# Kernel tuning notes

Measured on AMD Instinct MI355X. Metric: run time of the kernel, lower is better.

## Reference

```python
import jax, jax.numpy as jnp
import numpy as np

DIM = 1024
N_HEADS = 16
HEAD_DIM = DIM // N_HEADS


def setup_inputs() -> dict:
    key = jax.random.key(0)
    k1, k2, k3 = jax.random.split(key, 3)
    x = jax.random.normal(k1, (1, 4096, DIM), dtype=jnp.float32)
    # nn.Linear weights stored as [out, in]; y = x @ W.T
    w_qkv = jax.random.normal(k2, (3 * DIM, DIM), dtype=jnp.float32) * (DIM ** -0.5)
    w_o = jax.random.normal(k3, (DIM, DIM), dtype=jnp.float32) * (DIM ** -0.5)
    return {"x": x, "w_qkv": w_qkv, "w_o": w_o}


def reference(x, w_qkv, w_o):
    b, s, _ = x.shape
    qkv = jnp.einsum('bsd,ed->bse', x, w_qkv)  # [b, s, 3*dim]
    qkv = qkv.reshape(b, s, 3, N_HEADS, HEAD_DIM)
    qkv = jnp.transpose(qkv, (2, 0, 3, 1, 4))  # [3, b, h, s, hd]
    q, k, v = qkv[0], qkv[1], qkv[2]
    scale = HEAD_DIM ** -0.5
    scores = jnp.einsum('bhqd,bhkd->bhqk', q, k) * scale  # full O(N^2) scores
    attn = jax.nn.softmax(scores, axis=-1)
    out = jnp.einsum('bhqk,bhkd->bhqd', attn, v)
    out = jnp.transpose(out, (0, 2, 1, 3)).reshape(b, s, DIM)
    return jnp.einsum('bsd,ed->bse', out, w_o)
```

## Files before the change

kernel.cpp:

```cpp
#include <hip/hip_runtime.h>

typedef __bf16 bf16x8 __attribute__((ext_vector_type(8)));
typedef float f32x4 __attribute__((ext_vector_type(4)));
typedef unsigned short ushort_t;
typedef unsigned int uint_t;

constexpr int S = 4096, DMODEL = 1024, NH = 16, HD = 64;
#define QSCALE 0.18033688011112042f

#if __has_builtin(__builtin_amdgcn_exp2f)
#define EXP2(x) __builtin_amdgcn_exp2f(x)
#else
#define EXP2(x) exp2f(x)
#endif

__device__ inline ushort_t f2bf(float f) {
  uint_t u = __builtin_bit_cast(uint_t, f);
  u = u + 0x7FFFu + ((u >> 16) & 1u);
  return (ushort_t)(u >> 16);
}

__device__ inline ushort_t f2bf_hw(float f) {
  __bf16 h = (__bf16)f;
  return __builtin_bit_cast(ushort_t, h);
}

__device__ inline void gl2lds16(const ushort_t* g, ushort_t* l) {
  __builtin_amdgcn_global_load_lds(
      (const __attribute__((address_space(1))) unsigned int*)g,
      (__attribute__((address_space(3))) unsigned int*)l, 16, 0, 0);
}

__global__ __launch_bounds__(256) void cvt_f32_bf16(const float* __restrict__ in,
                                                    ushort_t* __restrict__ out, int n4) {
  int i = blockIdx.x * 256 + threadIdx.x;
  if (i >= n4) return;
  float4 f = reinterpret_cast<const float4*>(in)[i];
  ushort4 o;
  o.x = f2bf(f.x); o.y = f2bf(f.y); o.z = f2bf(f.z); o.w = f2bf(f.w);
  reinterpret_cast<ushort4*>(out)[i] = o;
}

template <int EPI>
__global__ __launch_bounds__(256) void gemm_bt(const ushort_t* __restrict__ A,
                                               const ushort_t* __restrict__ B,
                                               int M, int N, int K,
                                               float* __restrict__ Cf,
                                               ushort_t* __restrict__ qb,
                                               ushort_t* __restrict__ kb,
                                               ushort_t* __restrict__ vtb) {
  __shared__ ushort_t sA[128 * 64];
  __shared__ ushort_t sB[128 * 64];
  const int t = threadIdx.x;
  const int lane = t & 63, w = t >> 6;
  const int wr = w >> 1, wc = w & 1;
  const int rA0 = blockIdx.y * 128, rB0 = blockIdx.x * 128;

  f32x4 acc[4][4];
#pragma unroll
  for (int m = 0; m < 4; ++m)
#pragma unroll
    for (int n = 0; n < 4; ++n) acc[m][n] = (f32x4){0.f, 0.f, 0.f, 0.f};

  const int srow = t >> 3;
  const int scol = (t & 7) * 8;
  const int ldsbase = w * 512;

  for (int k0 = 0; k0 < K; k0 += 64) {
#pragma unroll
    for (int i = 0; i < 4; ++i) {
      int r = i * 32 + srow;
      int kc = scol ^ ((r & 7) << 3);
      gl2lds16(&A[(size_t)(rA0 + r) * K + k0 + kc], &sA[i * 2048 + ldsbase]);
    }
#pragma unroll
    for (int i = 0; i < 4; ++i) {
      int r = i * 32 + srow;
      int kc = scol ^ ((r & 7) << 3);
      gl2lds16(&B[(size_t)(rB0 + r) * K + k0 + kc], &sB[i * 2048 + ldsbase]);
    }
    __syncthreads();
#pragma unroll
    for (int ks = 0; ks < 2; ++ks) {
      const int kk = ks * 32 + (lane >> 4) * 8;
      bf16x8 af[4], bfr[4];
#pragma unroll
      for (int m = 0; m < 4; ++m) {
        int row = wr * 64 + m * 16 + (lane & 15);
        af[m] = *(const bf16x8*)&sA[row * 64 + (kk ^ ((row & 7) << 3))];
      }
#pragma unroll
      for (int n = 0; n < 4; ++n) {
        int row = wc * 64 + n * 16 + (lane & 15);
        bfr[n] = *(const bf16x8*)&sB[row * 64 + (kk ^ ((row & 7) << 3))];
      }
#pragma unroll
      for (int m = 0; m < 4; ++m)
#pragma unroll
        for (int n = 0; n < 4; ++n)
          acc[m][n] = __builtin_amdgcn_mfma_f32_16x16x32_bf16(af[m], bfr[n], acc[m][n], 0, 0, 0);
    }
    __syncthreads();
  }

#pragma unroll
  for (int m = 0; m < 4; ++m)
#pragma unroll
    for (int n = 0; n < 4; ++n)
#pragma unroll
      for (int r = 0; r < 4; ++r) {
        int row = rA0 + wr * 64 + m * 16 + (lane >> 4) * 4 + r;
        int col = rB0 + wc * 64 + n * 16 + (lane & 15);
        float v = acc[m][n][r];
        if constexpr (EPI == 0) {
          Cf[(size_t)row * N + col] = v;
        } else {
          int t3 = col >> 10, h = (col >> 6) & 15, d = col & 63;
          if (t3 == 0)      qb[((size_t)h * S + row) * HD + d] = f2bf_hw(v * QSCALE);
          else if (t3 == 1) kb[((size_t)h * S + row) * HD + d] = f2bf_hw(v);
          else              vtb[((size_t)h * HD + d) * S + row] = f2bf_hw(v);
        }
      }
}

__global__ __launch_bounds__(256) void gemm_bt_n64(const ushort_t* __restrict__ A,
                                                   const ushort_t* __restrict__ B,
                                                   int M, int N, int K,
                                                   float* __restrict__ Cf) {
  __shared__ ushort_t sA[128 * 64];
  __shared__ ushort_t sB[64 * 64];
  const int t = threadIdx.x;
  const int lane = t & 63, w = t >> 6;
  const int wr = w >> 1, wc = w & 1;
  const int rA0 = blockIdx.y * 128, rB0 = blockIdx.x * 64;

  f32x4 acc[4][2];
#pragma unroll
  for (int m = 0; m < 4; ++m)
#pragma unroll
    for (int n = 0; n < 2; ++n) acc[m][n] = (f32x4){0.f, 0.f, 0.f, 0.f};

  const int srow = t >> 3;
  const int scol = (t & 7) * 8;
  const int ldsbase = w * 512;

  for (int k0 = 0; k0 < K; k0 += 64) {
#pragma unroll
    for (int i = 0; i < 4; ++i) {
      int r = i * 32 + srow;
      int kc = scol ^ ((r & 7) << 3);
      gl2lds16(&A[(size_t)(rA0 + r) * K + k0 + kc], &sA[i * 2048 + ldsbase]);
    }
#pragma unroll
    for (int i = 0; i < 2; ++i) {
      int r = i * 32 + srow;
      int kc = scol ^ ((r & 7) << 3);
      gl2lds16(&B[(size_t)(rB0 + r) * K + k0 + kc], &sB[i * 2048 + ldsbase]);
    }
    __syncthreads();
#pragma unroll
    for (int ks = 0; ks < 2; ++ks) {
      const int kk = ks * 32 + (lane >> 4) * 8;
      bf16x8 af[4], bfr[2];
#pragma unroll
      for (int m = 0; m < 4; ++m) {
        int row = wr * 64 + m * 16 + (lane & 15);
        af[m] = *(const bf16x8*)&sA[row * 64 + (kk ^ ((row & 7) << 3))];
      }
#pragma unroll
      for (int n = 0; n < 2; ++n) {
        int row = wc * 32 + n * 16 + (lane & 15);
        bfr[n] = *(const bf16x8*)&sB[row * 64 + (kk ^ ((row & 7) << 3))];
      }
#pragma unroll
      for (int m = 0; m < 4; ++m)
#pragma unroll
        for (int n = 0; n < 2; ++n)
          acc[m][n] = __builtin_amdgcn_mfma_f32_16x16x32_bf16(af[m], bfr[n], acc[m][n], 0, 0, 0);
    }
    __syncthreads();
  }

#pragma unroll
  for (int m = 0; m < 4; ++m)
#pragma unroll
    for (int n = 0; n < 2; ++n)
#pragma unroll
      for (int r = 0; r < 4; ++r) {
        int row = rA0 + wr * 64 + m * 16 + (lane >> 4) * 4 + r;
        int col = rB0 + wc * 32 + n * 16 + (lane & 15);
        Cf[(size_t)row * N + col] = acc[m][n][r];
      }
}

__global__ __launch_bounds__(512) void attn_fwd(const ushort_t* __restrict__ qb,
                                                const ushort_t* __restrict__ kb,
                                                const ushort_t* __restrict__ vtb,
                                                ushort_t* __restrict__ aob) {
  __shared__ ushort_t sK[3][64 * 64];
  __shared__ ushort_t sV[3][64 * 64];
  __shared__ ushort_t sP[8][16 * 64];
  const int t = threadIdx.x, lane = t & 63, w = t >> 6;
  const int h = blockIdx.y;
  const int q0 = blockIdx.x * 128;
  const ushort_t* qh = qb + (size_t)h * S * HD;
  const ushort_t* kh = kb + (size_t)h * S * HD;
  const ushort_t* vh = vtb + (size_t)h * HD * S;

  bf16x8 qf[2];
  {
    int qr = q0 + w * 16 + (lane & 15);
    const ushort_t* p = &qh[(size_t)qr * HD + (lane >> 4) * 8];
    qf[0] = *(const bf16x8*)p;
    qf[1] = *(const bf16x8*)(p + 32);
  }
  f32x4 acc[4];
#pragma unroll
  for (int n = 0; n < 4; ++n) acc[n] = (f32x4){0.f, 0.f, 0.f, 0.f};
  float lsum[4] = {0.f, 0.f, 0.f, 0.f};

  const int srow = t >> 3;
  const int scol = (t & 7) * 8;
  const int kc = scol ^ ((srow & 7) << 3);
  const int ldsbase = w * 512;
  const int kk0 = (lane >> 4) * 8;

  auto stage = [&](int buf, int kv0) {
    gl2lds16(&kh[(size_t)(kv0 + srow) * HD + kc], &sK[buf][ldsbase]);
    gl2lds16(&vh[(size_t)srow * S + kv0 + kc], &sV[buf][ldsbase]);
  };

  constexpr int NT = S / 64;
  stage(0, 0);
  stage(1, 64);

  for (int ti = 0; ti < NT; ++ti) {
    const int buf = ti % 3;
    if (ti + 2 < NT) {
      stage((ti + 2) % 3, (ti + 2) * 64);
      asm volatile("s_waitcnt vmcnt(4)" ::: "memory");
    } else if (ti + 1 < NT) {
      asm volatile("s_waitcnt vmcnt(2)" ::: "memory");
    } else {
      asm volatile("s_waitcnt vmcnt(0)" ::: "memory");
    }
    __builtin_amdgcn_sched_barrier(0);
    __builtin_amdgcn_s_barrier();

    const ushort_t* Kb = &sK[buf][0];
    const ushort_t* Vb = &sV[buf][0];

    f32x4 sc[4];
    __builtin_amdgcn_s_setprio(1);
#pragma unroll
    for (int nt = 0; nt < 4; ++nt) {
      sc[nt] = (f32x4){0.f, 0.f, 0.f, 0.f};
      int row = nt * 16 + (lane & 15);
#pragma unroll
      for (int ks = 0; ks < 2; ++ks) {
        int kk = ks * 32 + kk0;
        bf16x8 kf = *(const bf16x8*)&Kb[row * 64 + (kk ^ ((row & 7) << 3))];
        sc[nt] = __builtin_amdgcn_mfma_f32_16x16x32_bf16(qf[ks], kf, sc[nt], 0, 0, 0);
      }
    }
    __builtin_amdgcn_s_setprio(0);

    float p[4][4];
#pragma unroll
    for (int r = 0; r < 4; ++r) {
      float ps = 0.f;
#pragma unroll
      for (int nt = 0; nt < 4; ++nt) {
        float pv = EXP2(sc[nt][r]);
        p[nt][r] = pv;
        ps += pv;
      }
      lsum[r] += ps;
    }
    const int prow_base = (lane >> 4) * 4;
#pragma unroll
    for (int nt = 0; nt < 4; ++nt) {
      int col = nt * 16 + (lane & 15);
#pragma unroll
      for (int r = 0; r < 4; ++r) {
        int row = prow_base + r;
        sP[w][row * 64 + (col ^ ((row & 7) << 3))] = f2bf_hw(p[nt][r]);
      }
    }
    bf16x8 pf[2];
    {
      int row = lane & 15;
#pragma unroll
      for (int ks = 0; ks < 2; ++ks) {
        int kk = ks * 32 + kk0;
        pf[ks] = *(const bf16x8*)&sP[w][row * 64 + (kk ^ ((row & 7) << 3))];
      }
    }
    __builtin_amdgcn_s_setprio(1);
#pragma unroll
    for (int nt = 0; nt < 4; ++nt) {
      int row = nt * 16 + (lane & 15);
#pragma unroll
      for (int ks = 0; ks < 2; ++ks) {
        int kk = ks * 32 + kk0;
        bf16x8 vf = *(const bf16x8*)&Vb[row * 64 + (kk ^ ((row & 7) << 3))];
        acc[nt] = __builtin_amdgcn_mfma_f32_16x16x32_bf16(pf[ks], vf, acc[nt], 0, 0, 0);
      }
    }
    __builtin_amdgcn_s_setprio(0);
    __builtin_amdgcn_s_barrier();
  }
  float linv[4];
#pragma unroll
  for (int r = 0; r < 4; ++r) {
    float l = lsum[r];
    l += __shfl_xor(l, 1);
    l += __shfl_xor(l, 2);
    l += __shfl_xor(l, 4);
    l += __shfl_xor(l, 8);
    linv[r] = 1.0f / l;
  }
#pragma unroll
  for (int nt = 0; nt < 4; ++nt)
#pragma unroll
    for (int r = 0; r < 4; ++r) {
      int row = q0 + w * 16 + (lane >> 4) * 4 + r;
      int col = h * HD + nt * 16 + (lane & 15);
      aob[(size_t)row * DMODEL + col] = f2bf_hw(acc[nt][r] * linv[r]);
    }
}

extern "C" void kernel_launch(void* const* d_in, const int* in_sizes, int n_in,
                              void* d_out, int out_size, void* d_ws, size_t ws_size,
                              hipStream_t stream) {
  const float* x = (const float*)d_in[0];
  const float* wqkv = (const float*)d_in[1];
  const float* wo = (const float*)d_in[2];
  float* out = (float*)d_out;
  char* ws = (char*)d_ws;
  const size_t MB = 1024ull * 1024ull;
  ushort_t* xb  = (ushort_t*)(ws);
  ushort_t* wqb = (ushort_t*)(ws + 8 * MB);
  ushort_t* wob = (ushort_t*)(ws + 14 * MB);
  ushort_t* qb  = (ushort_t*)(ws + 16 * MB);
  ushort_t* kb  = (ushort_t*)(ws + 24 * MB);
  ushort_t* vtb = (ushort_t*)(ws + 32 * MB);
  ushort_t* aob = (ushort_t*)(ws + 40 * MB);

  cvt_f32_bf16<<<(S * DMODEL / 4 + 255) / 256, 256, 0, stream>>>(x, xb, S * DMODEL / 4);
  cvt_f32_bf16<<<(3 * DMODEL * DMODEL / 4 + 255) / 256, 256, 0, stream>>>(wqkv, wqb, 3 * DMODEL * DMODEL / 4);
  cvt_f32_bf16<<<(DMODEL * DMODEL / 4 + 255) / 256, 256, 0, stream>>>(wo, wob, DMODEL * DMODEL / 4);

  dim3 g1(3 * DMODEL / 128, S / 128);
  gemm_bt<1><<<g1, 256, 0, stream>>>(xb, wqb, S, 3 * DMODEL, DMODEL, nullptr, qb, kb, vtb);

  dim3 ga(S / 128, NH);
  attn_fwd<<<ga, 512, 0, stream>>>(qb, kb, vtb, aob);

  dim3 g2(DMODEL / 64, S / 128);
  gemm_bt_n64<<<g2, 256, 0, stream>>>(aob, wob, S, DMODEL, DMODEL, out);
}
```

Before: 177.4 us.

## Load K fragments directly into registers, keep only V staged in LDS

The attention kernel stops staging K tiles through shared memory and instead has every wave load its K MFMA fragments straight from global memory into registers, prefetching the next tile right after the QK^T MFMAs. The vmcnt waits and barrier move to just before the PV stage and are retuned to count the outstanding K loads. This cuts LDS traffic and a barrier point, but each of the 8 waves now reads the full K tile from global/L2 itself, adds register pressure, and depends on hand-counted vmcnt values being correct.

```diff
diff --git a/kernel.cpp b/kernel.cpp
--- a/kernel.cpp
+++ b/kernel.cpp
@@ -197,7 +197,6 @@
                                                 const ushort_t* __restrict__ kb,
                                                 const ushort_t* __restrict__ vtb,
                                                 ushort_t* __restrict__ aob) {
-  __shared__ ushort_t sK[3][64 * 64];
   __shared__ ushort_t sV[3][64 * 64];
   __shared__ ushort_t sP[8][16 * 64];
   const int t = threadIdx.x, lane = t & 63, w = t >> 6;
@@ -207,10 +206,12 @@
   const ushort_t* kh = kb + (size_t)h * S * HD;
   const ushort_t* vh = vtb + (size_t)h * HD * S;
 
+  const int l15 = lane & 15, g = lane >> 4;
+  const int kk0 = g * 8;
+
   bf16x8 qf[2];
   {
-    int qr = q0 + w * 16 + (lane & 15);
-    const ushort_t* p = &qh[(size_t)qr * HD + (lane >> 4) * 8];
+    const ushort_t* p = &qh[(size_t)(q0 + w * 16 + l15) * HD + kk0];
     qf[0] = *(const bf16x8*)p;
     qf[1] = *(const bf16x8*)(p + 32);
   }
@@ -223,47 +224,42 @@
   const int scol = (t & 7) * 8;
   const int kc = scol ^ ((srow & 7) << 3);
   const int ldsbase = w * 512;
-  const int kk0 = (lane >> 4) * 8;
-
-  auto stage = [&](int buf, int kv0) {
-    gl2lds16(&kh[(size_t)(kv0 + srow) * HD + kc], &sK[buf][ldsbase]);
+
+  auto stageV = [&](int buf, int kv0) {
     gl2lds16(&vh[(size_t)srow * S + kv0 + kc], &sV[buf][ldsbase]);
   };
 
+  const ushort_t* kfbase = kh + (size_t)l15 * HD + kk0;
+  auto loadK = [&](bf16x8 kf[4][2], int kv0) {
+#pragma unroll
+    for (int nt = 0; nt < 4; ++nt)
+#pragma unroll
+      for (int ks = 0; ks < 2; ++ks)
+        kf[nt][ks] = *(const bf16x8*)(kfbase + (size_t)(kv0 + nt * 16) * HD + ks * 32);
+  };
+
   constexpr int NT = S / 64;
-  stage(0, 0);
-  stage(1, 64);
+  stageV(0, 0);
+  stageV(1, 64);
+  bf16x8 kf[4][2];
+  loadK(kf, 0);
 
   for (int ti = 0; ti < NT; ++ti) {
     const int buf = ti % 3;
-    if (ti + 2 < NT) {
-      stage((ti + 2) % 3, (ti + 2) * 64);
-      asm volatile("s_waitcnt vmcnt(4)" ::: "memory");
-    } else if (ti + 1 < NT) {
-      asm volatile("s_waitcnt vmcnt(2)" ::: "memory");
-    } else {
-      asm volatile("s_waitcnt vmcnt(0)" ::: "memory");
-    }
-    __builtin_amdgcn_sched_barrier(0);
-    __builtin_amdgcn_s_barrier();
-
-    const ushort_t* Kb = &sK[buf][0];
-    const ushort_t* Vb = &sV[buf][0];
+    if (ti + 2 < NT) stageV((ti + 2) % 3, (ti + 2) * 64);
 
     f32x4 sc[4];
     __builtin_amdgcn_s_setprio(1);
 #pragma unroll
     for (int nt = 0; nt < 4; ++nt) {
       sc[nt] = (f32x4){0.f, 0.f, 0.f, 0.f};
-      int row = nt * 16 + (lane & 15);
-#pragma unroll
-      for (int ks = 0; ks < 2; ++ks) {
-        int kk = ks * 32 + kk0;
-        bf16x8 kf = *(const bf16x8*)&Kb[row * 64 + (kk ^ ((row & 7) << 3))];
-        sc[nt] = __builtin_amdgcn_mfma_f32_16x16x32_bf16(qf[ks], kf, sc[nt], 0, 0, 0);
-      }
+#pragma unroll
+      for (int ks = 0; ks < 2; ++ks)
+        sc[nt] = __builtin_amdgcn_mfma_f32_16x16x32_bf16(qf[ks], kf[nt][ks], sc[nt], 0, 0, 0);
     }
     __builtin_amdgcn_s_setprio(0);
+
+    if (ti + 1 < NT) loadK(kf, (ti + 1) * 64);
 
     float p[4][4];
 #pragma unroll
@@ -277,10 +273,10 @@
       }
       lsum[r] += ps;
     }
-    const int prow_base = (lane >> 4) * 4;
+    const int prow_base = g * 4;
 #pragma unroll
     for (int nt = 0; nt < 4; ++nt) {
-      int col = nt * 16 + (lane & 15);
+      int col = nt * 16 + l15;
 #pragma unroll
       for (int r = 0; r < 4; ++r) {
         int row = prow_base + r;
@@ -288,22 +284,27 @@
       }
     }
     bf16x8 pf[2];
-    {
-      int row = lane & 15;
+#pragma unroll
+    for (int ks = 0; ks < 2; ++ks) {
+      int kk = ks * 32 + kk0;
+      pf[ks] = *(const bf16x8*)&sP[w][l15 * 64 + (kk ^ ((l15 & 7) << 3))];
+    }
+
+    if (ti == 0)           asm volatile("s_waitcnt vmcnt(18)" ::: "memory");
+    else if (ti < NT - 2)  asm volatile("s_waitcnt vmcnt(26)" ::: "memory");
+    else if (ti == NT - 2) asm volatile("s_waitcnt vmcnt(25)" ::: "memory");
+    else                   asm volatile("s_waitcnt vmcnt(16)" ::: "memory");
+    __builtin_amdgcn_sched_barrier(0);
+    __builtin_amdgcn_s_barrier();
+
+    __builtin_amdgcn_s_setprio(1);
+#pragma unroll
+    for (int nt = 0; nt < 4; ++nt) {
+      int row = nt * 16 + l15;
 #pragma unroll
       for (int ks = 0; ks < 2; ++ks) {
         int kk = ks * 32 + kk0;
-        pf[ks] = *(const bf16x8*)&sP[w][row * 64 + (kk ^ ((row & 7) << 3))];
-      }
-    }
-    __builtin_amdgcn_s_setprio(1);
-#pragma unroll
-    for (int nt = 0; nt < 4; ++nt) {
-      int row = nt * 16 + (lane & 15);
-#pragma unroll
-      for (int ks = 0; ks < 2; ++ks) {
-        int kk = ks * 32 + kk0;
-        bf16x8 vf = *(const bf16x8*)&Vb[row * 64 + (kk ^ ((row & 7) << 3))];
+        bf16x8 vf = *(const bf16x8*)&sV[buf][row * 64 + (kk ^ ((row & 7) << 3))];
         acc[nt] = __builtin_amdgcn_mfma_f32_16x16x32_bf16(pf[ks], vf, acc[nt], 0, 0, 0);
       }
     }
@@ -324,8 +325,8 @@
   for (int nt = 0; nt < 4; ++nt)
 #pragma unroll
     for (int r = 0; r < 4; ++r) {
-      int row = q0 + w * 16 + (lane >> 4) * 4 + r;
-      int col = h * HD + nt * 16 + (lane & 15);
+      int row = q0 + w * 16 + g * 4 + r;
+      int col = h * HD + nt * 16 + l15;
       aob[(size_t)row * DMODEL + col] = f2bf_hw(acc[nt][r] * linv[r]);
     }
 }
```

Result: slower. 319.1 us (+79.8%).
